# Optimization experiments

Hardware: AMD Instinct MI355X
Metric: run time of the kernel (lower is better)

Reference implementation:

```python
import jax, jax.numpy as jnp
import numpy as np

B, S, E, H, L, V = 64, 512, 256, 256, 5, 50001  # vocab_size+1 rows, padding_idx=0
GC = 256  # gcn_hidden
NC = [10, 5]


def lstm_dir(x, Wih, Whh, b):
    # x: [B,S,D]; Wih: [4H,D]; Whh: [4H,H]; b: [4H] (= b_ih + b_hh)
    h0 = jnp.zeros((x.shape[0], Whh.shape[1]), x.dtype)
    def step(carry, xt):
        h, c = carry
        g = xt @ Wih.T + h @ Whh.T + b
        i, f, gg, o = jnp.split(g, 4, axis=-1)  # torch gate order i,f,g,o
        c = jax.nn.sigmoid(f) * c + jax.nn.sigmoid(i) * jnp.tanh(gg)
        h = jax.nn.sigmoid(o) * jnp.tanh(c)
        return (h, c), h
    _, hs = jax.lax.scan(step, (h0, h0), jnp.swapaxes(x, 0, 1))
    return jnp.swapaxes(hs, 0, 1)  # [B,S,H]


def layer_norm(x, g, b, eps=1e-5):
    mu = jnp.mean(x, -1, keepdims=True)
    var = jnp.mean((x - mu) ** 2, -1, keepdims=True)
    return (x - mu) * jax.lax.rsqrt(var + eps) * g + b


def banded_adj_matmul(x, mask):
    # adj has only super/sub-diagonal ones, masked by m_i*m_j, row-normalized (+1e-8).
    m = mask
    m_next = jnp.pad(m[:, 1:], ((0, 0), (0, 1)))
    m_prev = jnp.pad(m[:, :-1], ((0, 0), (1, 0)))
    rs = m * (m_prev + m_next) + 1e-8  # row sums
    c_next = (m * m_next / rs)[:, :, None]
    c_prev = (m * m_prev / rs)[:, :, None]
    x_next = jnp.pad(x[:, 1:], ((0, 0), (0, 1), (0, 0)))
    x_prev = jnp.pad(x[:, :-1], ((0, 0), (1, 0), (0, 0)))
    return c_next * x_next + c_prev * x_prev


def gcn_layer(x, mask, W, b, gamma, beta):
    h = banded_adj_matmul(x, mask)
    h = h @ W.T + b
    h = h + x  # in_dim == out_dim -> residual
    return jax.nn.relu(layer_norm(h, gamma, beta))


def setup_inputs() -> dict:
    key = jax.random.key(0)
    ks = jax.random.split(key, 24)
    rn = lambda k, sh, s=0.05: jax.random.normal(k, sh, jnp.float32) * s
    seq = jax.random.randint(ks[0], (B, S), 0, V, jnp.int32)
    mask = jnp.ones((B, S), jnp.float32)
    aux = rn(ks[1], (B, 6), 1.0)
    emb_table = rn(ks[2], (V, E), 0.1).at[0].set(0.0)  # padding_idx=0
    Wih0 = rn(ks[3], (2, 4 * H, E))
    Whh0 = rn(ks[4], (2, 4 * H, H))
    b0 = rn(ks[5], (2, 4 * H))
    Wih = rn(ks[6], (L - 1, 2, 4 * H, 2 * H))
    Whh = rn(ks[7], (L - 1, 2, 4 * H, H))
    bL = rn(ks[8], (L - 1, 2, 4 * H))
    gcn_W = rn(ks[9], (3, GC, E))
    gcn_b = rn(ks[10], (3, GC))
    gcn_gamma = jnp.ones((3, GC), jnp.float32)
    gcn_beta = jnp.zeros((3, GC), jnp.float32)
    fusion = 2 * H + GC + 6
    fc1_W = rn(ks[11], (512, fusion))
    fc1_b = rn(ks[12], (512,))
    fc2_W = rn(ks[13], (256, 512))
    fc2_b = rn(ks[14], (256,))
    head0_W = rn(ks[15], (NC[0], 256))
    head0_b = rn(ks[16], (NC[0],))
    head1_W = rn(ks[17], (NC[1], 256))
    head1_b = rn(ks[18], (NC[1],))
    return dict(seq=seq, mask=mask, aux=aux, emb_table=emb_table, Wih0=Wih0,
                Whh0=Whh0, b0=b0, Wih=Wih, Whh=Whh, bL=bL, gcn_W=gcn_W,
                gcn_b=gcn_b, gcn_gamma=gcn_gamma, gcn_beta=gcn_beta,
                fc1_W=fc1_W, fc1_b=fc1_b, fc2_W=fc2_W, fc2_b=fc2_b,
                head0_W=head0_W, head0_b=head0_b, head1_W=head1_W, head1_b=head1_b)


def reference(seq, mask, aux, emb_table, Wih0, Whh0, b0, Wih, Whh, bL,
              gcn_W, gcn_b, gcn_gamma, gcn_beta, fc1_W, fc1_b, fc2_W, fc2_b,
              head0_W, head0_b, head1_W, head1_b):
    emb = emb_table[seq]  # [B,S,E]; dropout = identity (eval)
    # 5-layer bidirectional LSTM
    out = emb
    for l in range(L):
        wih, whh, b = (Wih0, Whh0, b0) if l == 0 else (Wih[l - 1], Whh[l - 1], bL[l - 1])
        fwd = lstm_dir(out, wih[0], whh[0], b[0])
        bwd = jnp.flip(lstm_dir(jnp.flip(out, 1), wih[1], whh[1], b[1]), 1)
        out = jnp.concatenate([fwd, bwd], -1)  # [B,S,2H]
    lstm_out = out * mask[:, :, None]
    denom = jnp.clip(jnp.sum(mask, 1, keepdims=True), 1e-8)
    lstm_feat = jnp.sum(lstm_out, 1) / denom  # [B,2H]
    # GCN stack over banded adjacency
    g = emb
    for i in range(3):
        g = gcn_layer(g, mask, gcn_W[i], gcn_b[i], gcn_gamma[i], gcn_beta[i])
    g = g * mask[:, :, None]
    gcn_feat = jnp.sum(g, 1) / denom  # [B,GC]
    fused = jnp.concatenate([lstm_feat, gcn_feat, aux], 1)
    s = jax.nn.relu(fused @ fc1_W.T + fc1_b)
    s = jax.nn.relu(s @ fc2_W.T + fc2_b)
    return (s @ head0_W.T + head0_b, s @ head1_W.T + head1_b)
```

## Files before the change

kernel.cpp:

```cpp
#include <hip/hip_runtime.h>
#include <stdint.h>
#include <stddef.h>

typedef __bf16 bf16;
typedef __bf16 bf16x8 __attribute__((ext_vector_type(8)));
typedef __bf16 bf16x4 __attribute__((ext_vector_type(4)));
typedef float  f32x4  __attribute__((ext_vector_type(4)));
typedef int    v4i    __attribute__((ext_vector_type(4)));

#define NB   64
#define NS   512
#define NE   256
#define NH   256
#define NL   5
#define NGC  256
#define FUSION 774

__device__ __forceinline__ float sigm(float x) {
    return __fdividef(1.f, 1.f + __expf(-x));
}
__device__ __forceinline__ float tanh_(float x) {
    return __fdividef(2.f, 1.f + __expf(-2.f * x)) - 1.f;
}

__device__ __forceinline__ void gload_lds16(const void* g, void* l) {
    __builtin_amdgcn_global_load_lds(
        (const __attribute__((address_space(1))) void*)g,
        (__attribute__((address_space(3))) void*)l,
        16, 0, 0);
}

__global__ void k_cvt(const float* __restrict__ src, bf16* __restrict__ dst, int n4) {
    int i = blockIdx.x * 256 + threadIdx.x;
    if (i >= n4) return;
    f32x4 v = ((const f32x4*)src)[i];
    bf16x4 o;
    o[0] = (bf16)v[0]; o[1] = (bf16)v[1]; o[2] = (bf16)v[2]; o[3] = (bf16)v[3];
    ((bf16x4*)dst)[i] = o;
}

__global__ void k_cvt_perm(const float* __restrict__ src, bf16* __restrict__ dst,
                           int K, int nrows) {
    int r = blockIdx.x * 4 + (threadIdx.x >> 6);
    int lane = threadIdx.x & 63;
    if (r >= nrows) return;
    int g = r & 3, j = (r >> 2) & 255;
    int srcrow = (r & ~1023) | (g << 8) | j;
    const float* s = src + (size_t)srcrow * K;
    bf16* dp = dst + (size_t)r * K;
    for (int c = lane * 4; c < K; c += 256) {
        f32x4 v = *(const f32x4*)(s + c);
        bf16x4 o;
        o[0] = (bf16)v[0]; o[1] = (bf16)v[1]; o[2] = (bf16)v[2]; o[3] = (bf16)v[3];
        *(bf16x4*)(dp + c) = o;
    }
}

__global__ void k_perm_bias(const float* __restrict__ b0, const float* __restrict__ bL,
                            float* __restrict__ pb) {
    int i = blockIdx.x * 256 + threadIdx.x;
    int r = i & 2047;
    int layer = i >> 11;
    int g = r & 3, j = (r >> 2) & 255, dh = r >> 10;
    int srcidx = dh * 1024 + g * 256 + j;
    float v = (layer == 0) ? b0[srcidx] : bL[(size_t)(layer - 1) * 2048 + srcidx];
    pb[i] = v;
}

__global__ void k_embed(const int* __restrict__ seq, const float* __restrict__ table,
                        float* __restrict__ ef, bf16* __restrict__ eb) {
    int t  = blockIdx.x * 256 + threadIdx.x;
    int bs = t >> 6;
    int c4 = (t & 63) << 2;
    int row = seq[bs];
    f32x4 v = *(const f32x4*)(table + (size_t)row * NE + c4);
    *(f32x4*)(ef + (size_t)bs * NE + c4) = v;
    bf16x4 o;
    o[0] = (bf16)v[0]; o[1] = (bf16)v[1]; o[2] = (bf16)v[2]; o[3] = (bf16)v[3];
    *(bf16x4*)(eb + (size_t)bs * NE + c4) = o;
}

__global__ __launch_bounds__(256, 2)
void k_gemm(const bf16* __restrict__ A, const bf16* __restrict__ W,
            const float* __restrict__ bias, void* __restrict__ Cout,
            int M, int N, int K, int out_mode) {
    __shared__ __align__(16) bf16 sA[128 * 64];
    __shared__ __align__(16) bf16 sB[128 * 64];
    const int mblk = M >> 7, nblk = N >> 7;
    int bid = blockIdx.x;
    int bm, bn;
    if ((mblk & 7) == 0) {
        int xcd = bid & 7, r = bid >> 3;
        int bmo = r / nblk;
        bm = xcd * (mblk >> 3) + bmo;
        bn = r - bmo * nblk;
    } else {
        bm = bid % mblk;
        bn = bid / mblk;
    }
    int m0 = bm << 7, n0 = bn << 7;
    int tid  = threadIdx.x;
    int wave = tid >> 6, lane = tid & 63;
    int wm = wave >> 1, wn = wave & 1;
    int l15 = lane & 15, quad = lane >> 4;

    f32x4 acc[4][4] = {};

    const int r0 = tid >> 3;
    const int c0 = (tid & 7) * 8;
    const bf16* Ab = A + (size_t)(m0 + r0) * K + c0;
    const bf16* Wb = W + (size_t)(n0 + r0) * K + c0;
    bf16* sAd = sA + tid * 8;
    bf16* sBd = sB + tid * 8;

    for (int k0 = 0; k0 < K; k0 += 64) {
#pragma unroll
        for (int i = 0; i < 4; i++) {
            gload_lds16(Ab + (size_t)(i * 32) * K + k0, sAd + i * 2048);
            gload_lds16(Wb + (size_t)(i * 32) * K + k0, sBd + i * 2048);
        }
        __syncthreads();
#pragma unroll
        for (int kk = 0; kk < 2; kk++) {
            bf16x8 af[4], bfr[4];
#pragma unroll
            for (int mt = 0; mt < 4; mt++)
                af[mt] = *(const bf16x8*)(sA + (wm * 64 + mt * 16 + l15) * 64 + kk * 32 + quad * 8);
#pragma unroll
            for (int nt = 0; nt < 4; nt++)
                bfr[nt] = *(const bf16x8*)(sB + (wn * 64 + nt * 16 + l15) * 64 + kk * 32 + quad * 8);
#pragma unroll
            for (int mt = 0; mt < 4; mt++)
#pragma unroll
                for (int nt = 0; nt < 4; nt++)
                    acc[mt][nt] = __builtin_amdgcn_mfma_f32_16x16x32_bf16(af[mt], bfr[nt], acc[mt][nt], 0, 0, 0);
        }
        __syncthreads();
    }
#pragma unroll
    for (int mt = 0; mt < 4; mt++) {
#pragma unroll
        for (int nt = 0; nt < 4; nt++) {
            int col = n0 + wn * 64 + nt * 16 + l15;
            float bv = bias[col];
            int row0 = m0 + wm * 64 + mt * 16 + quad * 4;
#pragma unroll
            for (int r4 = 0; r4 < 4; r4++) {
                float v = acc[mt][nt][r4] + bv;
                int r = row0 + r4;
                if (out_mode == 1) {
                    ((bf16*)Cout)[(size_t)r * N + col] = (bf16)v;
                } else {
                    ((float*)Cout)[(size_t)r * N + col] = v;
                }
            }
        }
    }
}

__global__ __launch_bounds__(256, 2)
void k_gcn_fused(const bf16* __restrict__ A,
                 const bf16* __restrict__ W,
                 const float* __restrict__ bias,
                 const float* __restrict__ x,
                 const float* __restrict__ gamma, const float* __restrict__ beta,
                 float* __restrict__ outx)
{
    __shared__ __align__(16) bf16 sA[128 * 64];
    __shared__ __align__(16) bf16 sB[2][128 * 64];
    __shared__ float lnred[2][128][2];
    const int m0 = blockIdx.x << 7;
    int tid = threadIdx.x;
    int wave = tid >> 6, lane = tid & 63;
    int wm = wave >> 1, wn = wave & 1;
    int l15 = lane & 15, quad = lane >> 4;

    f32x4 acc[2][4][4] = {};

    const int r0 = tid >> 3;
    const int c0 = (tid & 7) * 8;
    const bf16* Ab = A + (size_t)(m0 + r0) * 256 + c0;
    const bf16* Wb = W + (size_t)r0 * 256 + c0;
    bf16* sAd = sA + tid * 8;

    for (int k0 = 0; k0 < 256; k0 += 64) {
#pragma unroll
        for (int i = 0; i < 4; i++) {
            gload_lds16(Ab + (size_t)(i * 32) * 256 + k0, sAd + i * 2048);
            gload_lds16(Wb + (size_t)(i * 32) * 256 + k0, sB[0] + tid * 8 + i * 2048);
            gload_lds16(Wb + (size_t)(128 + i * 32) * 256 + k0, sB[1] + tid * 8 + i * 2048);
        }
        __syncthreads();
#pragma unroll
        for (int kk = 0; kk < 2; kk++) {
            bf16x8 af[4];
#pragma unroll
            for (int mt = 0; mt < 4; mt++)
                af[mt] = *(const bf16x8*)(sA + (wm * 64 + mt * 16 + l15) * 64 + kk * 32 + quad * 8);
#pragma unroll
            for (int bn = 0; bn < 2; bn++) {
                bf16x8 bfr[4];
#pragma unroll
                for (int nt = 0; nt < 4; nt++)
                    bfr[nt] = *(const bf16x8*)(sB[bn] + (wn * 64 + nt * 16 + l15) * 64 + kk * 32 + quad * 8);
#pragma unroll
                for (int mt = 0; mt < 4; mt++)
#pragma unroll
                    for (int nt = 0; nt < 4; nt++)
                        acc[bn][mt][nt] = __builtin_amdgcn_mfma_f32_16x16x32_bf16(af[mt], bfr[nt], acc[bn][mt][nt], 0, 0, 0);
            }
        }
        __syncthreads();
    }

    float psum[4][4], psq[4][4];
#pragma unroll
    for (int mt = 0; mt < 4; mt++)
#pragma unroll
        for (int r4 = 0; r4 < 4; r4++) { psum[mt][r4] = 0.f; psq[mt][r4] = 0.f; }

#pragma unroll
    for (int bn = 0; bn < 2; bn++)
#pragma unroll
        for (int nt = 0; nt < 4; nt++) {
            int col = bn * 128 + wn * 64 + nt * 16 + l15;
            float bv = bias[col];
#pragma unroll
            for (int mt = 0; mt < 4; mt++) {
                int row0 = m0 + wm * 64 + mt * 16 + quad * 4;
#pragma unroll
                for (int r4 = 0; r4 < 4; r4++) {
                    float v = acc[bn][mt][nt][r4] + bv + x[(size_t)(row0 + r4) * 256 + col];
                    acc[bn][mt][nt][r4] = v;
                    psum[mt][r4] += v;
                    psq[mt][r4]  += v * v;
                }
            }
        }
#pragma unroll
    for (int mt = 0; mt < 4; mt++)
#pragma unroll
        for (int r4 = 0; r4 < 4; r4++) {
#pragma unroll
            for (int off = 8; off >= 1; off >>= 1) {
                psum[mt][r4] += __shfl_xor(psum[mt][r4], off);
                psq[mt][r4]  += __shfl_xor(psq[mt][r4], off);
            }
        }
    if (l15 == 0) {
#pragma unroll
        for (int mt = 0; mt < 4; mt++)
#pragma unroll
            for (int r4 = 0; r4 < 4; r4++) {
                int rl = wm * 64 + mt * 16 + quad * 4 + r4;
                lnred[wn][rl][0] = psum[mt][r4];
                lnred[wn][rl][1] = psq[mt][r4];
            }
    }
    __syncthreads();
#pragma unroll
    for (int mt = 0; mt < 4; mt++) {
        int rl0 = wm * 64 + mt * 16 + quad * 4;
#pragma unroll
        for (int r4 = 0; r4 < 4; r4++) {
            float s  = lnred[0][rl0 + r4][0] + lnred[1][rl0 + r4][0];
            float sq = lnred[0][rl0 + r4][1] + lnred[1][rl0 + r4][1];
            float mu = s * (1.f / 256.f);
            float var = sq * (1.f / 256.f) - mu * mu;
            psum[mt][r4] = mu;
            psq[mt][r4]  = rsqrtf(var + 1e-5f);
        }
    }
#pragma unroll
    for (int bn = 0; bn < 2; bn++)
#pragma unroll
        for (int nt = 0; nt < 4; nt++) {
            int col = bn * 128 + wn * 64 + nt * 16 + l15;
            float gv = gamma[col], bv2 = beta[col];
#pragma unroll
            for (int mt = 0; mt < 4; mt++) {
                int row0 = m0 + wm * 64 + mt * 16 + quad * 4;
#pragma unroll
                for (int r4 = 0; r4 < 4; r4++) {
                    float y = (acc[bn][mt][nt][r4] - psum[mt][r4]) * psq[mt][r4] * gv + bv2;
                    outx[(size_t)(row0 + r4) * 256 + col] = fmaxf(y, 0.f);
                }
            }
        }
}

__global__ void k_prep_i8(const float* __restrict__ Whh0, const float* __restrict__ WhhL,
                          signed char* __restrict__ Wp8, float* __restrict__ scales) {
    int gw = blockIdx.x * 4 + (threadIdx.x >> 6);
    int lane = threadIdx.x & 63;
    int row = gw & 1023;
    int d = (gw >> 10) & 1;
    int layer = gw >> 11;
    const float* src = (layer == 0)
        ? (Whh0 + ((size_t)d * 1024 + row) * 256)
        : (WhhL + (((size_t)(layer - 1) * 2 + d) * 1024 + row) * 256);
    f32x4 v = *(const f32x4*)(src + lane * 4);
    float am = fmaxf(fmaxf(fabsf(v[0]), fabsf(v[1])), fmaxf(fabsf(v[2]), fabsf(v[3])));
#pragma unroll
    for (int off = 32; off >= 1; off >>= 1) am = fmaxf(am, __shfl_xor(am, off));
    am = fmaxf(am, 1e-8f);
    float inv = 127.f / am;
    int q0 = (int)__builtin_rintf(v[0] * inv);
    int q1 = (int)__builtin_rintf(v[1] * inv);
    int q2 = (int)__builtin_rintf(v[2] * inv);
    int q3 = (int)__builtin_rintf(v[3] * inv);
    uint32_t packed = (q0 & 255) | ((q1 & 255) << 8) | ((q2 & 255) << 16) | ((q3 & 255) << 24);
    int g = row >> 8, rem = row & 255;
    int w = rem >> 4, l15r = rem & 15;
    int k = lane * 4;
    int kt = k >> 6, q = (k >> 4) & 3, j = k & 15;
    size_t cell = ((size_t)layer * 2 + d) * 256 + (w * 4 + g) * 4 + kt;
    *(uint32_t*)(Wp8 + cell * 1024 + (q * 16 + l15r) * 16 + j) = packed;
    if (lane == 0)
        scales[((size_t)layer * 2 + d) * 1024 + row] = am * (1.f / (127.f * 127.f));
}

__global__ __launch_bounds__(512, 2)
void k_lstm_i8(const bf16* __restrict__ G,
               const signed char* __restrict__ Wp8,
               const float* __restrict__ sc,
               bf16* __restrict__ io_out)
{
    __shared__ signed char hs[2][2 * 4 * 80];

    const int d   = blockIdx.x & 1;
    const int bg  = blockIdx.x >> 1;
    const int tid = threadIdx.x;
    const int w = tid >> 6, lane = tid & 63;
    const int l15 = lane & 15, quad = lane >> 4;
    const int b_loc = quad & 1;
    const int jg    = quad >> 1;
    const int b = bg * 2 + b_loc;
    const int j = (w + jg * 8) * 16 + l15;

    v4i Wr[2][4][4];
#pragma unroll
    for (int sl = 0; sl < 2; sl++) {
        const int ws = w + sl * 8;
        const signed char* wb = Wp8 + ((size_t)d * 256 + ws * 16) * 1024 + lane * 16;
#pragma unroll
        for (int g = 0; g < 4; g++)
#pragma unroll
            for (int kt = 0; kt < 4; kt++)
                Wr[sl][g][kt] = *(const v4i*)(wb + (g * 4 + kt) * 1024);
    }
#pragma unroll
    for (int sl = 0; sl < 2; sl++)
#pragma unroll
        for (int g = 0; g < 4; g++)
#pragma unroll
            for (int kt = 0; kt < 4; kt++)
                asm volatile("" : "+v"(Wr[sl][g][kt]));

    float scv[4];
#pragma unroll
    for (int g = 0; g < 4; g++)
        scv[g] = sc[d * 1024 + g * 256 + j];

    const bf16* gbase = G + d * 1024 + j * 4;
    const size_t iob = (size_t)b * NS * 512 + d * 256 + j;

    const int hwr = (b_loc * 4 + (j >> 6)) * 80 + (j & 63);
    const int hrd = (((l15 >> 2) & 1) * 4 + (l15 & 3)) * 80 + quad * 16;
    const int rr = l15 & 3;

    float cst = 0.f;

    bf16x4 gcur = *(const bf16x4*)(gbase + (size_t)(b * 512 + (d ? (NS - 1) : 0)) * 2048);
    bf16x4 gnxt = *(const bf16x4*)(gbase + (size_t)(b * 512 + (d ? (NS - 2) : 1)) * 2048);

    {
        bf16x4 gfut = *(const bf16x4*)(gbase + (size_t)(b * 512 + (d ? (NS - 3) : 2)) * 2048);
        float pi = (float)gcur[0];
        float pg = (float)gcur[2], po = (float)gcur[3];
        float ig = sigm(pi), gc = tanh_(pg), og = sigm(po);
        float c = ig * gc;
        cst = c;
        float hh = og * tanh_(c);
        const int tcur = d ? (NS - 1) : 0;
        io_out[iob + (size_t)tcur * 512] = (bf16)hh;
        hs[0][hwr] = (signed char)(int)__builtin_rintf(hh * 127.f);
        gcur = gnxt; gnxt = gfut;
        asm volatile("s_waitcnt lgkmcnt(0)" ::: "memory");
        __builtin_amdgcn_s_barrier();
        asm volatile("" ::: "memory");
    }

    for (int t = 1; t < NS; t++) {
        const int rb = (t + 1) & 1, wbuf = t & 1;

        bf16x4 gfut = gcur;
        if (t + 2 < NS) {
            const int tt2 = d ? (NS - 3 - t) : (t + 2);
            gfut = *(const bf16x4*)(gbase + (size_t)(b * 512 + tt2) * 2048);
        }

        v4i acc[2][4] = {};
        {
            v4i chunk = *(const v4i*)&hs[rb][hrd];
            v4i a[4];
#pragma unroll
            for (int kt = 0; kt < 4; kt++) {
                a[kt][0] = (rr == kt) ? chunk[0] : 0;
                a[kt][1] = (rr == kt) ? chunk[1] : 0;
                a[kt][2] = (rr == kt) ? chunk[2] : 0;
                a[kt][3] = (rr == kt) ? chunk[3] : 0;
            }
#pragma unroll
            for (int sl = 0; sl < 2; sl++)
#pragma unroll
                for (int g = 0; g < 4; g++)
#pragma unroll
                    for (int kt = 0; kt < 4; kt++)
                        acc[sl][g] = __builtin_amdgcn_mfma_i32_16x16x64_i8(a[kt], Wr[sl][g][kt], acc[sl][g], 0, 0, 0);
        }

        int s[4];
#pragma unroll
        for (int g = 0; g < 4; g++) {
            int s0 = acc[0][g][0] + acc[0][g][1] + acc[0][g][2] + acc[0][g][3];
            int s1 = acc[1][g][0] + acc[1][g][1] + acc[1][g][2] + acc[1][g][3];
            s[g] = jg ? s1 : s0;
        }
        float pi = (float)s[0] * scv[0] + (float)gcur[0];
        float pf = (float)s[1] * scv[1] + (float)gcur[1];
        float pg = (float)s[2] * scv[2] + (float)gcur[2];
        float po = (float)s[3] * scv[3] + (float)gcur[3];
        float ig = sigm(pi), fg = sigm(pf), gc = tanh_(pg), og = sigm(po);
        float c = fg * cst + ig * gc;
        cst = c;
        float hh = og * tanh_(c);
        const int tcur = d ? (NS - 1 - t) : t;
        io_out[iob + (size_t)tcur * 512] = (bf16)hh;
        hs[wbuf][hwr] = (signed char)(int)__builtin_rintf(hh * 127.f);

        gcur = gnxt; gnxt = gfut;

        asm volatile("s_waitcnt lgkmcnt(0)" ::: "memory");
        __builtin_amdgcn_s_barrier();
        asm volatile("" ::: "memory");
    }
}

__global__ void k_banded(const float* __restrict__ x, const float* __restrict__ mask,
                         bf16* __restrict__ outb) {
    int t  = blockIdx.x * 256 + threadIdx.x;
    int bs = t >> 6;
    int c4 = (t & 63) << 2;
    int s = bs & (NS - 1);
    float m  = mask[bs];
    float mn = (s < NS - 1) ? mask[bs + 1] : 0.f;
    float mp = (s > 0)      ? mask[bs - 1] : 0.f;
    float rs = m * (mp + mn) + 1e-8f;
    float cn = m * mn / rs;
    float cp = m * mp / rs;
    f32x4 vn = {}, vp = {};
    if (s < NS - 1) vn = *(const f32x4*)(x + (size_t)(bs + 1) * NGC + c4);
    if (s > 0)      vp = *(const f32x4*)(x + (size_t)(bs - 1) * NGC + c4);
    bf16x4 o;
#pragma unroll
    for (int i = 0; i < 4; i++) o[i] = (bf16)(cn * vn[i] + cp * vp[i]);
    *(bf16x4*)(outb + (size_t)bs * NGC + c4) = o;
}

__global__ void k_pool_bf16(const bf16* __restrict__ src, const float* __restrict__ mask,
                            float* __restrict__ feat) {
    int b = blockIdx.x, f = threadIdx.x;
    float acc = 0.f, dm = 0.f;
    for (int t = 0; t < NS; t++) {
        float m = mask[b * NS + t];
        acc += m * (float)src[((size_t)b * NS + t) * 512 + f];
        dm += m;
    }
    feat[b * 512 + f] = acc / fmaxf(dm, 1e-8f);
}
__global__ void k_pool_f32(const float* __restrict__ src, const float* __restrict__ mask,
                           float* __restrict__ feat) {
    int b = blockIdx.x, f = threadIdx.x;
    float acc = 0.f, dm = 0.f;
    for (int t = 0; t < NS; t++) {
        float m = mask[b * NS + t];
        acc += m * src[((size_t)b * NS + t) * NGC + f];
        dm += m;
    }
    feat[b * NGC + f] = acc / fmaxf(dm, 1e-8f);
}

__global__ __launch_bounds__(512)
void k_head(const float* __restrict__ lfeat, const float* __restrict__ gfeat,
            const float* __restrict__ aux,
            const float* __restrict__ fc1W, const float* __restrict__ fc1b,
            const float* __restrict__ fc2W, const float* __restrict__ fc2b,
            const float* __restrict__ h0W, const float* __restrict__ h0b,
            const float* __restrict__ h1W, const float* __restrict__ h1b,
            float* __restrict__ out) {
    __shared__ float fused[FUSION];
    __shared__ float s1[512];
    __shared__ float s2[256];
    int m = blockIdx.x, tid = threadIdx.x;
    if (tid < 512) fused[tid] = lfeat[m * 512 + tid];
    if (tid < 256) fused[512 + tid] = gfeat[m * 256 + tid];
    if (tid < 6)   fused[768 + tid] = aux[m * 6 + tid];
    __syncthreads();
    {
        float a = fc1b[tid];
        const float* w = fc1W + (size_t)tid * FUSION;
        for (int k = 0; k < FUSION; k++) a += w[k] * fused[k];
        s1[tid] = fmaxf(a, 0.f);
    }
    __syncthreads();
    if (tid < 256) {
        float a = fc2b[tid];
        const float* w = fc2W + (size_t)tid * 512;
        for (int k = 0; k < 512; k++) a += w[k] * s1[k];
        s2[tid] = fmaxf(a, 0.f);
    }
    __syncthreads();
    if (tid < 15) {
        if (tid < 10) {
            float a = h0b[tid];
            const float* w = h0W + (size_t)tid * 256;
            for (int k = 0; k < 256; k++) a += w[k] * s2[k];
            out[m * 10 + tid] = a;
        } else {
            int n = tid - 10;
            float a = h1b[n];
            const float* w = h1W + (size_t)n * 256;
            for (int k = 0; k < 256; k++) a += w[k] * s2[k];
            out[640 + m * 5 + n] = a;
        }
    }
}

extern "C" void kernel_launch(void* const* d_in, const int* in_sizes, int n_in,
                              void* d_out, int out_size, void* d_ws, size_t ws_size,
                              hipStream_t stream) {
    const int*   seq   = (const int*)d_in[0];
    const float* mask  = (const float*)d_in[1];
    const float* aux   = (const float*)d_in[2];
    const float* table = (const float*)d_in[3];
    const float* Wih0  = (const float*)d_in[4];
    const float* Whh0  = (const float*)d_in[5];
    const float* b0    = (const float*)d_in[6];
    const float* WihL  = (const float*)d_in[7];
    const float* WhhL  = (const float*)d_in[8];
    const float* bL    = (const float*)d_in[9];
    const float* gcnW  = (const float*)d_in[10];
    const float* gcnb  = (const float*)d_in[11];
    const float* gcnG  = (const float*)d_in[12];
    const float* gcnBe = (const float*)d_in[13];
    const float* fc1W  = (const float*)d_in[14];
    const float* fc1b  = (const float*)d_in[15];
    const float* fc2W  = (const float*)d_in[16];
    const float* fc2b  = (const float*)d_in[17];
    const float* h0W   = (const float*)d_in[18];
    const float* h0b   = (const float*)d_in[19];
    const float* h1W   = (const float*)d_in[20];
    const float* h1b   = (const float*)d_in[21];
    float* outp = (float*)d_out;

    char* ws = (char*)d_ws;
    const size_t MROWS = (size_t)NB * NS;
    signed char* Wp8 = (signed char*)(ws + 0);
    float* wsc     = (float*)(ws + 2621440);
    bf16*  Wbf     = (bf16*) (ws + 2662400);
    bf16*  wb0     = Wbf;
    bf16*  wbL     = Wbf + 524288;
    bf16*  wgcn    = Wbf + 524288 + 4194304;
    bf16*  emb_b   = (bf16*) (ws + 33554432);
    bf16*  io0     = (bf16*) (ws + 50331648);
    bf16*  io1     = (bf16*) (ws + 83886080);
    char*  Greg    =          ws + 117440512;
    bf16*  G       = (bf16*)  Greg;
    float* lfeat   = (float*)(ws + 251658240);
    float* gfeat   = (float*)(ws + 251789312);
    float* pbias   = (float*)(ws + 251854848);
    float* gcnA  = (float*)(Greg + 0);
    float* gcnB_ = (float*)(Greg + 33554432);
    bf16*  gtmp  = (bf16*) (Greg + 100663296);
    (void)ws_size; (void)n_in; (void)in_sizes; (void)out_size;

    k_cvt_perm<<<dim3(512),  dim3(256), 0, stream>>>(Wih0, wb0, 256, 2048);
    k_cvt_perm<<<dim3(2048), dim3(256), 0, stream>>>(WihL, wbL, 512, 8192);
    k_perm_bias<<<dim3(40), dim3(256), 0, stream>>>(b0, bL, pbias);
    k_cvt<<<dim3(192),  dim3(256), 0, stream>>>(gcnW, wgcn, 49152);
    k_prep_i8<<<dim3(2560), dim3(256), 0, stream>>>(Whh0, WhhL, Wp8, wsc);

    k_embed<<<dim3(8192), dim3(256), 0, stream>>>(seq, table, gcnA, emb_b);

    const float* xcur = gcnA;
    float* xnxt[3] = {gcnB_, gcnA, gcnB_};
    for (int i = 0; i < 3; i++) {
        k_banded<<<dim3(8192), dim3(256), 0, stream>>>(xcur, mask, gtmp);
        k_gcn_fused<<<dim3(MROWS / 128), dim3(256), 0, stream>>>(
            gtmp, wgcn + (size_t)i * NGC * NGC, gcnb + i * NGC, xcur,
            gcnG + i * NGC, gcnBe + i * NGC, xnxt[i]);
        xcur = xnxt[i];
    }
    k_pool_f32<<<dim3(NB), dim3(NGC), 0, stream>>>(xcur, mask, gfeat);

    const bf16* Xin = emb_b;
    int Kin = NE;
    bf16* ios[2] = {io0, io1};
    for (int l = 0; l < NL; l++) {
        const bf16* wih = l ? (wbL + (size_t)(l - 1) * 1048576) : wb0;
        k_gemm<<<dim3((MROWS / 128) * (2048 / 128)), dim3(256), 0, stream>>>(
            Xin, wih, pbias + (size_t)l * 2048, G, (int)MROWS, 2048, Kin, 1);
        bf16* lio = ios[l & 1];
        k_lstm_i8<<<dim3(64), dim3(512), 0, stream>>>(
            G, Wp8 + (size_t)l * 524288, wsc + (size_t)l * 2048, lio);
        Xin = lio;
        Kin = 512;
    }
    k_pool_bf16<<<dim3(NB), dim3(512), 0, stream>>>(ios[(NL - 1) & 1], mask, lfeat);

    k_head<<<dim3(NB), dim3(512), 0, stream>>>(
        lfeat, gfeat, aux, fc1W, fc1b, fc2W, fc2b, h0W, h0b, h1W, h1b, outp);
}
```

Measured before the change: 3.170 ms.

## Overlap LSTM input-projection GEMM with recurrence via per-chunk flags

Splits each layer's input-projection GEMM by time chunk. A first kernel computes the first and last 128-step chunks, which the forward and backward directions need first. A fused kernel then runs the 64 recurrent LSTM blocks next to GEMM blocks that compute the middle chunks, and the GEMM blocks publish completion through atomic flags. LSTM blocks spin-wait on those flags just before they reach a chunk, so most GEMM work hides behind the serial recurrence. The GEMM tile also moves to 512 threads per block. The scheme depends on the LSTM blocks being resident before the GEMM blocks, and it uses a bounded spin as a deadlock guard.

After: 3.671 ms. 1.16x slower.

```diff
diff --git a/kernel.cpp b/kernel.cpp
--- a/kernel.cpp
+++ b/kernel.cpp
@@ -80,57 +80,36 @@
     *(bf16x4*)(eb + (size_t)bs * NE + c4) = o;
 }
 
-__global__ __launch_bounds__(256, 2)
-void k_gemm(const bf16* __restrict__ A, const bf16* __restrict__ W,
-            const float* __restrict__ bias, void* __restrict__ Cout,
-            int M, int N, int K, int out_mode) {
-    __shared__ __align__(16) bf16 sA[128 * 64];
-    __shared__ __align__(16) bf16 sB[128 * 64];
-    const int mblk = M >> 7, nblk = N >> 7;
-    int bid = blockIdx.x;
-    int bm, bn;
-    if ((mblk & 7) == 0) {
-        int xcd = bid & 7, r = bid >> 3;
-        int bmo = r / nblk;
-        bm = xcd * (mblk >> 3) + bmo;
-        bn = r - bmo * nblk;
-    } else {
-        bm = bid % mblk;
-        bn = bid / mblk;
-    }
-    int m0 = bm << 7, n0 = bn << 7;
-    int tid  = threadIdx.x;
+__device__ __forceinline__ void gemm_tile512(
+    const bf16* __restrict__ A, const bf16* __restrict__ W,
+    const float* __restrict__ bias, bf16* __restrict__ G,
+    int K, int m0, int n0, bf16* sA, bf16* sB)
+{
+    int tid = threadIdx.x;
     int wave = tid >> 6, lane = tid & 63;
     int wm = wave >> 1, wn = wave & 1;
     int l15 = lane & 15, quad = lane >> 4;
-
-    f32x4 acc[4][4] = {};
-
+    f32x4 acc[2][4] = {};
     const int r0 = tid >> 3;
     const int c0 = (tid & 7) * 8;
-    const bf16* Ab = A + (size_t)(m0 + r0) * K + c0;
-    const bf16* Wb = W + (size_t)(n0 + r0) * K + c0;
-    bf16* sAd = sA + tid * 8;
-    bf16* sBd = sB + tid * 8;
-
     for (int k0 = 0; k0 < K; k0 += 64) {
 #pragma unroll
-        for (int i = 0; i < 4; i++) {
-            gload_lds16(Ab + (size_t)(i * 32) * K + k0, sAd + i * 2048);
-            gload_lds16(Wb + (size_t)(i * 32) * K + k0, sBd + i * 2048);
+        for (int i = 0; i < 2; i++) {
+            gload_lds16(A + (size_t)(m0 + i * 64 + r0) * K + k0 + c0, sA + (i * 512 + tid) * 8);
+            gload_lds16(W + (size_t)(n0 + i * 64 + r0) * K + k0 + c0, sB + (i * 512 + tid) * 8);
         }
         __syncthreads();
 #pragma unroll
         for (int kk = 0; kk < 2; kk++) {
-            bf16x8 af[4], bfr[4];
-#pragma unroll
-            for (int mt = 0; mt < 4; mt++)
-                af[mt] = *(const bf16x8*)(sA + (wm * 64 + mt * 16 + l15) * 64 + kk * 32 + quad * 8);
+            bf16x8 af[2], bfr[4];
+#pragma unroll
+            for (int mt = 0; mt < 2; mt++)
+                af[mt] = *(const bf16x8*)(sA + (wm * 32 + mt * 16 + l15) * 64 + kk * 32 + quad * 8);
 #pragma unroll
             for (int nt = 0; nt < 4; nt++)
                 bfr[nt] = *(const bf16x8*)(sB + (wn * 64 + nt * 16 + l15) * 64 + kk * 32 + quad * 8);
 #pragma unroll
-            for (int mt = 0; mt < 4; mt++)
+            for (int mt = 0; mt < 2; mt++)
 #pragma unroll
                 for (int nt = 0; nt < 4; nt++)
                     acc[mt][nt] = __builtin_amdgcn_mfma_f32_16x16x32_bf16(af[mt], bfr[nt], acc[mt][nt], 0, 0, 0);
@@ -138,23 +117,221 @@
         __syncthreads();
     }
 #pragma unroll
-    for (int mt = 0; mt < 4; mt++) {
+    for (int mt = 0; mt < 2; mt++)
 #pragma unroll
         for (int nt = 0; nt < 4; nt++) {
             int col = n0 + wn * 64 + nt * 16 + l15;
             float bv = bias[col];
-            int row0 = m0 + wm * 64 + mt * 16 + quad * 4;
-#pragma unroll
-            for (int r4 = 0; r4 < 4; r4++) {
-                float v = acc[mt][nt][r4] + bv;
-                int r = row0 + r4;
-                if (out_mode == 1) {
-                    ((bf16*)Cout)[(size_t)r * N + col] = (bf16)v;
-                } else {
-                    ((float*)Cout)[(size_t)r * N + col] = v;
+            int row0 = m0 + wm * 32 + mt * 16 + quad * 4;
+#pragma unroll
+            for (int r4 = 0; r4 < 4; r4++)
+                G[(size_t)(row0 + r4) * 2048 + col] = (bf16)(acc[mt][nt][r4] + bv);
+        }
+}
+
+__global__ __launch_bounds__(512, 2)
+void k_gemm_lstm03(const bf16* __restrict__ A, const bf16* __restrict__ W,
+                   const float* __restrict__ bias, bf16* __restrict__ G, int K) {
+    __shared__ __align__(16) bf16 sA[128 * 64];
+    __shared__ __align__(16) bf16 sB[128 * 64];
+    int bn = blockIdx.x & 15;
+    int bmi = blockIdx.x >> 4;
+    int bm = (bmi >> 1) * 4 + ((bmi & 1) ? 3 : 0);
+    gemm_tile512(A, W, bias, G, K, bm << 7, bn << 7, sA, sB);
+}
+
+__global__ void k_prep_i8(const float* __restrict__ Whh0, const float* __restrict__ WhhL,
+                          signed char* __restrict__ Wp8, float* __restrict__ scales) {
+    int gw = blockIdx.x * 4 + (threadIdx.x >> 6);
+    int lane = threadIdx.x & 63;
+    int row = gw & 1023;
+    int d = (gw >> 10) & 1;
+    int layer = gw >> 11;
+    const float* src = (layer == 0)
+        ? (Whh0 + ((size_t)d * 1024 + row) * 256)
+        : (WhhL + (((size_t)(layer - 1) * 2 + d) * 1024 + row) * 256);
+    f32x4 v = *(const f32x4*)(src + lane * 4);
+    float am = fmaxf(fmaxf(fabsf(v[0]), fabsf(v[1])), fmaxf(fabsf(v[2]), fabsf(v[3])));
+#pragma unroll
+    for (int off = 32; off >= 1; off >>= 1) am = fmaxf(am, __shfl_xor(am, off));
+    am = fmaxf(am, 1e-8f);
+    float inv = 127.f / am;
+    int q0 = (int)__builtin_rintf(v[0] * inv);
+    int q1 = (int)__builtin_rintf(v[1] * inv);
+    int q2 = (int)__builtin_rintf(v[2] * inv);
+    int q3 = (int)__builtin_rintf(v[3] * inv);
+    uint32_t packed = (q0 & 255) | ((q1 & 255) << 8) | ((q2 & 255) << 16) | ((q3 & 255) << 24);
+    int g = row >> 8, rem = row & 255;
+    int w = rem >> 4, l15r = rem & 15;
+    int k = lane * 4;
+    int kt = k >> 6, q = (k >> 4) & 3, j = k & 15;
+    size_t cell = ((size_t)layer * 2 + d) * 256 + (w * 4 + g) * 4 + kt;
+    *(uint32_t*)(Wp8 + cell * 1024 + (q * 16 + l15r) * 16 + j) = packed;
+    if (lane == 0)
+        scales[((size_t)layer * 2 + d) * 1024 + row] = am * (1.f / (127.f * 127.f));
+}
+
+__global__ __launch_bounds__(512, 1)
+void k_lstm_fused(const bf16* __restrict__ A, const bf16* __restrict__ W,
+                  const float* __restrict__ bias, bf16* __restrict__ G,
+                  const signed char* __restrict__ Wp8, const float* __restrict__ sc,
+                  bf16* __restrict__ io_out, unsigned int* __restrict__ flags, int K)
+{
+    __shared__ __align__(16) bf16 sA[3 * 128 * 64];
+    __shared__ __align__(16) bf16 sB[3 * 128 * 64];
+    __shared__ signed char hs[2][2 * 4 * 80];
+
+    if (blockIdx.x >= 64) {
+        int g = blockIdx.x - 64;
+        int bn = g & 15;
+        int bmi = g >> 4;
+        int bm = (bmi >> 1) * 4 + ((bmi & 1) ? 2 : 1);
+        gemm_tile512(A, W, bias, G, K, bm << 7, bn << 7, sA, sB);
+        __syncthreads();
+        if (threadIdx.x == 0) {
+            __threadfence();
+            __hip_atomic_fetch_add(flags + bm, 1u, __ATOMIC_RELEASE,
+                                   __HIP_MEMORY_SCOPE_AGENT);
+        }
+        return;
+    }
+
+    const int d   = blockIdx.x & 1;
+    const int bg  = blockIdx.x >> 1;
+    const int tid = threadIdx.x;
+    const int w = tid >> 6, lane = tid & 63;
+    const int l15 = lane & 15, quad = lane >> 4;
+    const int b_loc = quad & 1;
+    const int jg    = quad >> 1;
+    const int b = bg * 2 + b_loc;
+    const int j = (w + jg * 8) * 16 + l15;
+
+    v4i Wr[2][4][4];
+#pragma unroll
+    for (int sl = 0; sl < 2; sl++) {
+        const int ws = w + sl * 8;
+        const signed char* wb = Wp8 + ((size_t)d * 256 + ws * 16) * 1024 + lane * 16;
+#pragma unroll
+        for (int g = 0; g < 4; g++)
+#pragma unroll
+            for (int kt = 0; kt < 4; kt++)
+                Wr[sl][g][kt] = *(const v4i*)(wb + (g * 4 + kt) * 1024);
+    }
+#pragma unroll
+    for (int sl = 0; sl < 2; sl++)
+#pragma unroll
+        for (int g = 0; g < 4; g++)
+#pragma unroll
+            for (int kt = 0; kt < 4; kt++)
+                asm volatile("" : "+v"(Wr[sl][g][kt]));
+
+    float scv[4];
+#pragma unroll
+    for (int g = 0; g < 4; g++)
+        scv[g] = sc[d * 1024 + g * 256 + j];
+
+    const bf16* gbase = G + d * 1024 + j * 4;
+    const size_t iob = (size_t)b * NS * 512 + d * 256 + j;
+
+    const int hwr = (b_loc * 4 + (j >> 6)) * 80 + (j & 63);
+    const int hrd = (((l15 >> 2) & 1) * 4 + (l15 & 3)) * 80 + quad * 16;
+    const int rr = l15 & 3;
+
+    float cst = 0.f;
+
+    bf16x4 gcur = *(const bf16x4*)(gbase + (size_t)(b * 512 + (d ? (NS - 1) : 0)) * 2048);
+    bf16x4 gnxt = *(const bf16x4*)(gbase + (size_t)(b * 512 + (d ? (NS - 2) : 1)) * 2048);
+
+    {
+        bf16x4 gfut = *(const bf16x4*)(gbase + (size_t)(b * 512 + (d ? (NS - 3) : 2)) * 2048);
+        float pi = (float)gcur[0];
+        float pg = (float)gcur[2], po = (float)gcur[3];
+        float ig = sigm(pi), gc = tanh_(pg), og = sigm(po);
+        float c = ig * gc;
+        cst = c;
+        float hh = og * tanh_(c);
+        const int tcur = d ? (NS - 1) : 0;
+        io_out[iob + (size_t)tcur * 512] = (bf16)hh;
+        hs[0][hwr] = (signed char)(int)__builtin_rintf(hh * 127.f);
+        gcur = gnxt; gnxt = gfut;
+        asm volatile("s_waitcnt lgkmcnt(0)" ::: "memory");
+        __builtin_amdgcn_s_barrier();
+        asm volatile("" ::: "memory");
+    }
+
+    for (int t = 1; t < NS; t++) {
+        if ((t & 127) == 126 && t + 2 < NS) {
+            int ch = (d ? (NS - 3 - t) : (t + 2)) >> 7;
+            if (ch == 1 || ch == 2) {
+                if (tid == 0) {
+                    unsigned gd = 0;
+                    while (__hip_atomic_load(flags + ((bg * 2) * 4 + ch),
+                                             __ATOMIC_RELAXED, __HIP_MEMORY_SCOPE_AGENT) < 16u) {
+                        if (++gd > (1u << 28)) break;
+                    }
+                    gd = 0;
+                    while (__hip_atomic_load(flags + ((bg * 2 + 1) * 4 + ch),
+                                             __ATOMIC_RELAXED, __HIP_MEMORY_SCOPE_AGENT) < 16u) {
+                        if (++gd > (1u << 28)) break;
+                    }
                 }
+                __syncthreads();
+                __threadfence();
             }
         }
+
+        const int rb = (t + 1) & 1, wbuf = t & 1;
+
+        bf16x4 gfut = gcur;
+        if (t + 2 < NS) {
+            const int tt2 = d ? (NS - 3 - t) : (t + 2);
+            gfut = *(const bf16x4*)(gbase + (size_t)(b * 512 + tt2) * 2048);
+        }
+
+        v4i acc[2][4] = {};
+        {
+            v4i chunk = *(const v4i*)&hs[rb][hrd];
+            v4i a[4];
+#pragma unroll
+            for (int kt = 0; kt < 4; kt++) {
+                a[kt][0] = (rr == kt) ? chunk[0] : 0;
+                a[kt][1] = (rr == kt) ? chunk[1] : 0;
+                a[kt][2] = (rr == kt) ? chunk[2] : 0;
+                a[kt][3] = (rr == kt) ? chunk[3] : 0;
+            }
+#pragma unroll
+            for (int sl = 0; sl < 2; sl++)
+#pragma unroll
+                for (int g = 0; g < 4; g++)
+#pragma unroll
+                    for (int kt = 0; kt < 4; kt++)
+                        acc[sl][g] = __builtin_amdgcn_mfma_i32_16x16x64_i8(a[kt], Wr[sl][g][kt], acc[sl][g], 0, 0, 0);
+        }
+
+        int s[4];
+#pragma unroll
+        for (int g = 0; g < 4; g++) {
+            int s0 = acc[0][g][0] + acc[0][g][1] + acc[0][g][2] + acc[0][g][3];
+            int s1 = acc[1][g][0] + acc[1][g][1] + acc[1][g][2] + acc[1][g][3];
+            s[g] = jg ? s1 : s0;
+        }
+        float pi = (float)s[0] * scv[0] + (float)gcur[0];
+        float pf = (float)s[1] * scv[1] + (float)gcur[1];
+        float pg = (float)s[2] * scv[2] + (float)gcur[2];
+        float po = (float)s[3] * scv[3] + (float)gcur[3];
+        float ig = sigm(pi), fg = sigm(pf), gc = tanh_(pg), og = sigm(po);
+        float c = fg * cst + ig * gc;
+        cst = c;
+        float hh = og * tanh_(c);
+        const int tcur = d ? (NS - 1 - t) : t;
+        io_out[iob + (size_t)tcur * 512] = (bf16)hh;
+        hs[wbuf][hwr] = (signed char)(int)__builtin_rintf(hh * 127.f);
+
+        gcur = gnxt; gnxt = gfut;
+
+        asm volatile("s_waitcnt lgkmcnt(0)" ::: "memory");
+        __builtin_amdgcn_s_barrier();
+        asm volatile("" ::: "memory");
     }
 }
 
@@ -287,164 +464,6 @@
                 }
             }
         }
-}
-
-__global__ void k_prep_i8(const float* __restrict__ Whh0, const float* __restrict__ WhhL,
-                          signed char* __restrict__ Wp8, float* __restrict__ scales) {
-    int gw = blockIdx.x * 4 + (threadIdx.x >> 6);
-    int lane = threadIdx.x & 63;
-    int row = gw & 1023;
-    int d = (gw >> 10) & 1;
-    int layer = gw >> 11;
-    const float* src = (layer == 0)
-        ? (Whh0 + ((size_t)d * 1024 + row) * 256)
-        : (WhhL + (((size_t)(layer - 1) * 2 + d) * 1024 + row) * 256);
-    f32x4 v = *(const f32x4*)(src + lane * 4);
-    float am = fmaxf(fmaxf(fabsf(v[0]), fabsf(v[1])), fmaxf(fabsf(v[2]), fabsf(v[3])));
-#pragma unroll
-    for (int off = 32; off >= 1; off >>= 1) am = fmaxf(am, __shfl_xor(am, off));
-    am = fmaxf(am, 1e-8f);
-    float inv = 127.f / am;
-    int q0 = (int)__builtin_rintf(v[0] * inv);
-    int q1 = (int)__builtin_rintf(v[1] * inv);
-    int q2 = (int)__builtin_rintf(v[2] * inv);
-    int q3 = (int)__builtin_rintf(v[3] * inv);
-    uint32_t packed = (q0 & 255) | ((q1 & 255) << 8) | ((q2 & 255) << 16) | ((q3 & 255) << 24);
-    int g = row >> 8, rem = row & 255;
-    int w = rem >> 4, l15r = rem & 15;
-    int k = lane * 4;
-    int kt = k >> 6, q = (k >> 4) & 3, j = k & 15;
-    size_t cell = ((size_t)layer * 2 + d) * 256 + (w * 4 + g) * 4 + kt;
-    *(uint32_t*)(Wp8 + cell * 1024 + (q * 16 + l15r) * 16 + j) = packed;
-    if (lane == 0)
-        scales[((size_t)layer * 2 + d) * 1024 + row] = am * (1.f / (127.f * 127.f));
-}
-
-__global__ __launch_bounds__(512, 2)
-void k_lstm_i8(const bf16* __restrict__ G,
-               const signed char* __restrict__ Wp8,
-               const float* __restrict__ sc,
-               bf16* __restrict__ io_out)
-{
-    __shared__ signed char hs[2][2 * 4 * 80];
-
-    const int d   = blockIdx.x & 1;
-    const int bg  = blockIdx.x >> 1;
-    const int tid = threadIdx.x;
-    const int w = tid >> 6, lane = tid & 63;
-    const int l15 = lane & 15, quad = lane >> 4;
-    const int b_loc = quad & 1;
-    const int jg    = quad >> 1;
-    const int b = bg * 2 + b_loc;
-    const int j = (w + jg * 8) * 16 + l15;
-
-    v4i Wr[2][4][4];
-#pragma unroll
-    for (int sl = 0; sl < 2; sl++) {
-        const int ws = w + sl * 8;
-        const signed char* wb = Wp8 + ((size_t)d * 256 + ws * 16) * 1024 + lane * 16;
-#pragma unroll
-        for (int g = 0; g < 4; g++)
-#pragma unroll
-            for (int kt = 0; kt < 4; kt++)
-                Wr[sl][g][kt] = *(const v4i*)(wb + (g * 4 + kt) * 1024);
-    }
-#pragma unroll
-    for (int sl = 0; sl < 2; sl++)
-#pragma unroll
-        for (int g = 0; g < 4; g++)
-#pragma unroll
-            for (int kt = 0; kt < 4; kt++)
-                asm volatile("" : "+v"(Wr[sl][g][kt]));
-
-    float scv[4];
-#pragma unroll
-    for (int g = 0; g < 4; g++)
-        scv[g] = sc[d * 1024 + g * 256 + j];
-
-    const bf16* gbase = G + d * 1024 + j * 4;
-    const size_t iob = (size_t)b * NS * 512 + d * 256 + j;
-
-    const int hwr = (b_loc * 4 + (j >> 6)) * 80 + (j & 63);
-    const int hrd = (((l15 >> 2) & 1) * 4 + (l15 & 3)) * 80 + quad * 16;
-    const int rr = l15 & 3;
-
-    float cst = 0.f;
-
-    bf16x4 gcur = *(const bf16x4*)(gbase + (size_t)(b * 512 + (d ? (NS - 1) : 0)) * 2048);
-    bf16x4 gnxt = *(const bf16x4*)(gbase + (size_t)(b * 512 + (d ? (NS - 2) : 1)) * 2048);
-
-    {
-        bf16x4 gfut = *(const bf16x4*)(gbase + (size_t)(b * 512 + (d ? (NS - 3) : 2)) * 2048);
-        float pi = (float)gcur[0];
-        float pg = (float)gcur[2], po = (float)gcur[3];
-        float ig = sigm(pi), gc = tanh_(pg), og = sigm(po);
-        float c = ig * gc;
-        cst = c;
-        float hh = og * tanh_(c);
-        const int tcur = d ? (NS - 1) : 0;
-        io_out[iob + (size_t)tcur * 512] = (bf16)hh;
-        hs[0][hwr] = (signed char)(int)__builtin_rintf(hh * 127.f);
-        gcur = gnxt; gnxt = gfut;
-        asm volatile("s_waitcnt lgkmcnt(0)" ::: "memory");
-        __builtin_amdgcn_s_barrier();
-        asm volatile("" ::: "memory");
-    }
-
-    for (int t = 1; t < NS; t++) {
-        const int rb = (t + 1) & 1, wbuf = t & 1;
-
-        bf16x4 gfut = gcur;
-        if (t + 2 < NS) {
-            const int tt2 = d ? (NS - 3 - t) : (t + 2);
-            gfut = *(const bf16x4*)(gbase + (size_t)(b * 512 + tt2) * 2048);
-        }
-
-        v4i acc[2][4] = {};
-        {
-            v4i chunk = *(const v4i*)&hs[rb][hrd];
-            v4i a[4];
-#pragma unroll
-            for (int kt = 0; kt < 4; kt++) {
-                a[kt][0] = (rr == kt) ? chunk[0] : 0;
-                a[kt][1] = (rr == kt) ? chunk[1] : 0;
-                a[kt][2] = (rr == kt) ? chunk[2] : 0;
-                a[kt][3] = (rr == kt) ? chunk[3] : 0;
-            }
-#pragma unroll
-            for (int sl = 0; sl < 2; sl++)
-#pragma unroll
-                for (int g = 0; g < 4; g++)
-#pragma unroll
-                    for (int kt = 0; kt < 4; kt++)
-                        acc[sl][g] = __builtin_amdgcn_mfma_i32_16x16x64_i8(a[kt], Wr[sl][g][kt], acc[sl][g], 0, 0, 0);
-        }
-
-        int s[4];
-#pragma unroll
-        for (int g = 0; g < 4; g++) {
-            int s0 = acc[0][g][0] + acc[0][g][1] + acc[0][g][2] + acc[0][g][3];
-            int s1 = acc[1][g][0] + acc[1][g][1] + acc[1][g][2] + acc[1][g][3];
-            s[g] = jg ? s1 : s0;
-        }
-        float pi = (float)s[0] * scv[0] + (float)gcur[0];
-        float pf = (float)s[1] * scv[1] + (float)gcur[1];
-        float pg = (float)s[2] * scv[2] + (float)gcur[2];
-        float po = (float)s[3] * scv[3] + (float)gcur[3];
-        float ig = sigm(pi), fg = sigm(pf), gc = tanh_(pg), og = sigm(po);
-        float c = fg * cst + ig * gc;
-        cst = c;
-        float hh = og * tanh_(c);
-        const int tcur = d ? (NS - 1 - t) : t;
-        io_out[iob + (size_t)tcur * 512] = (bf16)hh;
-        hs[wbuf][hwr] = (signed char)(int)__builtin_rintf(hh * 127.f);
-
-        gcur = gnxt; gnxt = gfut;
-
-        asm volatile("s_waitcnt lgkmcnt(0)" ::: "memory");
-        __builtin_amdgcn_s_barrier();
-        asm volatile("" ::: "memory");
-    }
 }
 
 __global__ void k_banded(const float* __restrict__ x, const float* __restrict__ mask,
@@ -580,6 +599,7 @@
     float* lfeat   = (float*)(ws + 251658240);
     float* gfeat   = (float*)(ws + 251789312);
     float* pbias   = (float*)(ws + 251854848);
+    unsigned int* flags = (unsigned int*)(ws + 251895808);
     float* gcnA  = (float*)(Greg + 0);
     float* gcnB_ = (float*)(Greg + 33554432);
     bf16*  gtmp  = (bf16*) (Greg + 100663296);
@@ -590,6 +610,7 @@
     k_perm_bias<<<dim3(40), dim3(256), 0, stream>>>(b0, bL, pbias);
     k_cvt<<<dim3(192),  dim3(256), 0, stream>>>(gcnW, wgcn, 49152);
     k_prep_i8<<<dim3(2560), dim3(256), 0, stream>>>(Whh0, WhhL, Wp8, wsc);
+    hipMemsetAsync(flags, 0, 5 * 256 * sizeof(unsigned int), stream);
 
     k_embed<<<dim3(8192), dim3(256), 0, stream>>>(seq, table, gcnA, emb_b);
 
@@ -609,11 +630,13 @@
     bf16* ios[2] = {io0, io1};
     for (int l = 0; l < NL; l++) {
         const bf16* wih = l ? (wbL + (size_t)(l - 1) * 1048576) : wb0;
-        k_gemm<<<dim3((MROWS / 128) * (2048 / 128)), dim3(256), 0, stream>>>(
-            Xin, wih, pbias + (size_t)l * 2048, G, (int)MROWS, 2048, Kin, 1);
         bf16* lio = ios[l & 1];
-        k_lstm_i8<<<dim3(64), dim3(512), 0, stream>>>(
-            G, Wp8 + (size_t)l * 524288, wsc + (size_t)l * 2048, lio);
+        k_gemm_lstm03<<<dim3(2048), dim3(512), 0, stream>>>(
+            Xin, wih, pbias + (size_t)l * 2048, G, Kin);
+        k_lstm_fused<<<dim3(2112), dim3(512), 0, stream>>>(
+            Xin, wih, pbias + (size_t)l * 2048, G,
+            Wp8 + (size_t)l * 524288, wsc + (size_t)l * 2048, lio,
+            flags + (size_t)l * 256, Kin);
         Xin = lio;
         Kin = 512;
     }
```
